# Kernel tuning notes

Measured on AMD Instinct MI355X. Metric: run time of the kernel, lower is better.

Reference implementation:

```python
import jax, jax.numpy as jnp
import numpy as np

N_NODES = 50000
N_EDGES = 800000
VOCAB = 4096
EMB = 128
HID = 128


def glorot(key, shape):
    limit = float(np.sqrt(6.0 / (shape[0] + shape[1])))
    return jax.random.uniform(key, shape, jnp.float32, -limit, limit)


def setup_inputs() -> dict:
    key = jax.random.key(0)
    k = jax.random.split(key, 6)
    x = jax.random.randint(k[0], (N_NODES, 1), 0, VOCAB, dtype=jnp.int64)
    edge_index = jax.random.randint(k[1], (2, N_EDGES), 0, N_NODES, dtype=jnp.int64)
    # Embedding init: normal(0, dim^-0.5)
    emb = jax.random.normal(k[2], (VOCAB, EMB), jnp.float32) * (EMB ** -0.5)
    W1 = glorot(k[3], (EMB, 2 * HID))
    b1 = jnp.zeros((2 * HID,), jnp.float32)
    W2 = glorot(k[4], (2 * HID, HID))
    b2 = jnp.zeros((HID,), jnp.float32)
    return {"x": x, "edge_index": edge_index, "emb": emb,
            "W1": W1, "b1": b1, "W2": W2, "b2": b2}


def _gcn_conv(h, src, dst, norm, W, b):
    # PyG GCNConv: transform then degree-normalized aggregate over A + I.
    h = h @ W                                   # [N, F_out]
    msg = norm[:, None] * h[src]                # [(E+N), F_out] gather
    out = jax.ops.segment_sum(msg, dst, num_segments=N_NODES)  # scatter-add
    return out + b


def _edges_with_self_loops_and_norm(edge_index):
    loop = jnp.arange(N_NODES, dtype=edge_index.dtype)
    src = jnp.concatenate([edge_index[0], loop])
    dst = jnp.concatenate([edge_index[1], loop])
    deg = jax.ops.segment_sum(jnp.ones_like(dst, jnp.float32), dst,
                              num_segments=N_NODES)
    inv_sqrt = jnp.where(deg > 0, deg ** -0.5, 0.0)
    norm = inv_sqrt[src] * inv_sqrt[dst]        # [(E+N)]
    return src, dst, norm


def reference(x, edge_index, emb, W1, b1, W2, b2):
    src, dst, norm = _edges_with_self_loops_and_norm(edge_index)
    h = emb[x[:, 0]]                            # embedding lookup + squeeze(1)
    h = jax.nn.relu(_gcn_conv(h, src, dst, norm, W1, b1))
    h = _gcn_conv(h, src, dst, norm, W2, b2)
    return h
```

## Files before the change

kernel.cpp:

```cpp
#include <hip/hip_runtime.h>


constexpr int FEAT = 128;
constexpr int HID2 = 256;
constexpr int CAP  = 64;

typedef __attribute__((ext_vector_type(8))) __bf16 bf16x8;
typedef __attribute__((ext_vector_type(4))) float f32x4;
typedef __attribute__((ext_vector_type(8))) _Float16 f16x8;
union FragU { uint4 u; bf16x8 b; };
union H16 { _Float16 f; unsigned short u; };

__device__ inline void split_bf16_rne(float v, unsigned short& h, unsigned short& l) {
  unsigned u = __float_as_uint(v);
  unsigned short hh = (unsigned short)((u + 0x7FFFu + ((u >> 16) & 1u)) >> 16);
  float r = v - __uint_as_float(((unsigned)hh) << 16);
  unsigned u2 = __float_as_uint(r);
  unsigned short ll = (unsigned short)((u2 + 0x7FFFu + ((u2 >> 16) & 1u)) >> 16);
  h = hh; l = ll;
}

__device__ inline void split_trunc1(float v, unsigned short& h, unsigned short& l) {
  unsigned u = __float_as_uint(v);
  h = (unsigned short)(u >> 16);
  float r = v - __uint_as_float(u & 0xFFFF0000u);
  l = (unsigned short)(__float_as_uint(r) >> 16);
}


__global__ __launch_bounds__(256) void k_init_prep(int* cnt, int N, int nblkN,
    const float* __restrict__ W1, const float* __restrict__ W2,
    unsigned short* __restrict__ w1s_hi, unsigned short* __restrict__ w1s_lo,
    unsigned short* __restrict__ w2s_hi, unsigned short* __restrict__ w2s_lo) {
  int b = blockIdx.x;
  if (b < nblkN) {
    int i = b * 256 + threadIdx.x;
    if (i < N) cnt[i] = 0;
    return;
  }
  int idx = (b - nblkN) * 256 + threadIdx.x;
  unsigned short h, l;
  if (idx < FEAT * HID2) {
    int k = idx >> 8, n = idx & 255;
    split_bf16_rne(W1[idx], h, l);
    int t = n >> 4, lr = n & 15, kc = k >> 5, quad = (k >> 3) & 3, j = k & 7;
    int us = (((t * 4 + kc) * 64 + quad * 16 + lr) << 3) + j;
    w1s_hi[us] = h;
    w1s_lo[us] = l;
  } else {
    int jj = idx - FEAT * HID2;
    int k = jj >> 7, n = jj & 127;
    split_bf16_rne(W2[jj], h, l);
    int t = n >> 4, lr = n & 15, kc = k >> 5, quad = (k >> 3) & 3, j = k & 7;
    int us = (((t * 8 + kc) * 64 + quad * 16 + lr) << 3) + j;
    w2s_hi[us] = h;
    w2s_lo[us] = l;
  }
}


__global__ __launch_bounds__(256) void k_bucket(const int* __restrict__ src,
    const int* __restrict__ dst, int* cnt, unsigned short* csr, int E, int chunkN) {
  int g = blockIdx.x & 7;
  int e = (blockIdx.x >> 3) * 256 + threadIdx.x;
  if (e >= E) return;
  int d = dst[e];
  int lo = g * chunkN;
  if (d >= lo && d < lo + chunkN) {
    int pos = atomicAdd(&cnt[d], 1);
    if (pos < CAP) csr[d * CAP + pos] = (unsigned short)src[e];
  }
}


__global__ __launch_bounds__(512, 2) void k_gmlp(
    const int* __restrict__ x, const float* __restrict__ emb,
    const int* __restrict__ cnt, const unsigned short* __restrict__ csr,
    const uint4* __restrict__ w1s_hi, const uint4* __restrict__ w1s_lo,
    const uint4* __restrict__ w2s_hi, const uint4* __restrict__ w2s_lo,
    const float* __restrict__ b1,
    unsigned short* __restrict__ hs2h, int N, int Np) {
  __shared__ __align__(16) unsigned short h1h[32 * 256];
  __shared__ __align__(16) unsigned short h1l[32 * 256];
  unsigned short* aggh = h1h;
  unsigned short* aggl = h1l;

  int tid  = threadIdx.x;
  int wave = tid >> 6, lane = tid & 63, quad = lane >> 4, lr = lane & 15;
  int bid  = blockIdx.x;
  int m0 = bid * 32;
  int rot1 = bid & 1;
  int kh0  = (bid >> 1) & 1;

  int glr = tid >> 4;
  int rt_g = glr >> 4, r15 = glr & 15;
  int c4  = (tid & 15) * 4;
  int kcg = c4 >> 5, qdg = (c4 >> 3) & 3, sub = c4 & 7;
  int L   = qdg * 16 + r15;
  int posL = L ^ ((L >> 4) & 3);

  {
    int node = m0 + glr;
    int fA = rt_g * 4 + kcg, fB = fA + 2;
    int pos = posL ^ ((fA & 1) << 2);
    int usA = ((fA * 64 + pos) << 3) + sub;
    int usB = ((fB * 64 + pos) << 3) + sub;
    if (node < N) {
      int degN = cnt[node];
      float wd = rsqrtf((float)(degN + 1));
      int deg = degN > CAP ? CAP : degN;

      const float* e0 = &emb[(long long)x[node] * FEAT + c4];
      float4 aA = *reinterpret_cast<const float4*>(e0);
      float4 aB = *reinterpret_cast<const float4*>(e0 + 64);
      aA.x *= wd; aA.y *= wd; aA.z *= wd; aA.w *= wd;
      aB.x *= wd; aB.y *= wd; aB.z *= wd; aB.w *= wd;

      const unsigned short* row = csr + node * CAP;
      int j = 0;
      for (; j + 7 < deg; j += 8) {
        uint4 c8 = *reinterpret_cast<const uint4*>(row + j);
        int s[8] = {(int)(c8.x & 0xFFFF), (int)(c8.x >> 16),
                    (int)(c8.y & 0xFFFF), (int)(c8.y >> 16),
                    (int)(c8.z & 0xFFFF), (int)(c8.z >> 16),
                    (int)(c8.w & 0xFFFF), (int)(c8.w >> 16)};
        const float* p[8];
        #pragma unroll
        for (int q = 0; q < 8; ++q) p[q] = &emb[(long long)x[s[q]] * FEAT + c4];
        float ws[8];
        #pragma unroll
        for (int q = 0; q < 8; ++q) ws[q] = rsqrtf((float)(cnt[s[q]] + 1));
        float4 rA[8], rB[8];
        #pragma unroll
        for (int q = 0; q < 8; ++q) {
          rA[q] = *reinterpret_cast<const float4*>(p[q]);
          rB[q] = *reinterpret_cast<const float4*>(p[q] + 64);
        }
        #pragma unroll
        for (int q = 0; q < 8; ++q) {
          aA.x += ws[q] * rA[q].x; aA.y += ws[q] * rA[q].y;
          aA.z += ws[q] * rA[q].z; aA.w += ws[q] * rA[q].w;
          aB.x += ws[q] * rB[q].x; aB.y += ws[q] * rB[q].y;
          aB.z += ws[q] * rB[q].z; aB.w += ws[q] * rB[q].w;
        }
      }
      if (j + 3 < deg) {
        uint2 c4e = *reinterpret_cast<const uint2*>(row + j);
        int s[4] = {(int)(c4e.x & 0xFFFF), (int)(c4e.x >> 16),
                    (int)(c4e.y & 0xFFFF), (int)(c4e.y >> 16)};
        const float* p[4];
        #pragma unroll
        for (int q = 0; q < 4; ++q) p[q] = &emb[(long long)x[s[q]] * FEAT + c4];
        float ws[4];
        #pragma unroll
        for (int q = 0; q < 4; ++q) ws[q] = rsqrtf((float)(cnt[s[q]] + 1));
        float4 rA[4], rB[4];
        #pragma unroll
        for (int q = 0; q < 4; ++q) {
          rA[q] = *reinterpret_cast<const float4*>(p[q]);
          rB[q] = *reinterpret_cast<const float4*>(p[q] + 64);
        }
        #pragma unroll
        for (int q = 0; q < 4; ++q) {
          aA.x += ws[q] * rA[q].x; aA.y += ws[q] * rA[q].y;
          aA.z += ws[q] * rA[q].z; aA.w += ws[q] * rA[q].w;
          aB.x += ws[q] * rB[q].x; aB.y += ws[q] * rB[q].y;
          aB.z += ws[q] * rB[q].z; aB.w += ws[q] * rB[q].w;
        }
        j += 4;
      }
      for (; j < deg; ++j) {
        int s = row[j];
        float w = rsqrtf((float)(cnt[s] + 1));
        const float* p = &emb[(long long)x[s] * FEAT + c4];
        float4 a = *reinterpret_cast<const float4*>(p);
        float4 b = *reinterpret_cast<const float4*>(p + 64);
        aA.x += w * a.x; aA.y += w * a.y; aA.z += w * a.z; aA.w += w * a.w;
        aB.x += w * b.x; aB.y += w * b.y; aB.z += w * b.z; aB.w += w * b.w;
      }

      aA.x *= wd; aA.y *= wd; aA.z *= wd; aA.w *= wd;
      aB.x *= wd; aB.y *= wd; aB.z *= wd; aB.w *= wd;
      ushort4 hA, lA, hB, lB;
      split_bf16_rne(aA.x, hA.x, lA.x);
      split_bf16_rne(aA.y, hA.y, lA.y);
      split_bf16_rne(aA.z, hA.z, lA.z);
      split_bf16_rne(aA.w, hA.w, lA.w);
      split_bf16_rne(aB.x, hB.x, lB.x);
      split_bf16_rne(aB.y, hB.y, lB.y);
      split_bf16_rne(aB.z, hB.z, lB.z);
      split_bf16_rne(aB.w, hB.w, lB.w);
      *reinterpret_cast<ushort4*>(aggh + usA) = hA;
      *reinterpret_cast<ushort4*>(aggl + usA) = lA;
      *reinterpret_cast<ushort4*>(aggh + usB) = hB;
      *reinterpret_cast<ushort4*>(aggl + usB) = lB;
    } else {
      ushort4 z = {0, 0, 0, 0};
      *reinterpret_cast<ushort4*>(aggh + usA) = z;
      *reinterpret_cast<ushort4*>(aggl + usA) = z;
      *reinterpret_cast<ushort4*>(aggh + usB) = z;
      *reinterpret_cast<ushort4*>(aggl + usB) = z;
    }
  }

  FragU bh[2][4], bl[2][4];
  auto loadB1 = [&](int t, int buf) {
    #pragma unroll
    for (int kc = 0; kc < 4; ++kc) {
      bh[buf][kc].u = w1s_hi[(t * 4 + kc) * 64 + lane];
      bl[buf][kc].u = w1s_lo[(t * 4 + kc) * 64 + lane];
    }
  };
  int t0 = wave * 2;
  loadB1(t0 + rot1, 0);

  __syncthreads();

  FragU a1h[2][4], a1l[2][4];
  {
    int posR = lane ^ ((lane >> 4) & 3);
    #pragma unroll
    for (int rt = 0; rt < 2; ++rt)
      #pragma unroll
      for (int kc = 0; kc < 4; ++kc) {
        int f = rt * 4 + kc;
        int us = ((f * 64 + (posR ^ ((f & 1) << 2))) << 3);
        a1h[rt][kc].u = *reinterpret_cast<const uint4*>(aggh + us);
        a1l[rt][kc].u = *reinterpret_cast<const uint4*>(aggl + us);
      }
  }

  __syncthreads();

  auto comp1 = [&](int t, int buf) {
    f32x4 hh[2], hl[2], lh[2];
    #pragma unroll
    for (int rt = 0; rt < 2; ++rt) {
      hh[rt] = f32x4{0.f, 0.f, 0.f, 0.f};
      hl[rt] = f32x4{0.f, 0.f, 0.f, 0.f};
      lh[rt] = f32x4{0.f, 0.f, 0.f, 0.f};
    }
    #pragma unroll
    for (int kc = 0; kc < 4; ++kc)
      #pragma unroll
      for (int rt = 0; rt < 2; ++rt) {
        hh[rt] = __builtin_amdgcn_mfma_f32_16x16x32_bf16(a1h[rt][kc].b, bh[buf][kc].b, hh[rt], 0, 0, 0);
        hl[rt] = __builtin_amdgcn_mfma_f32_16x16x32_bf16(a1h[rt][kc].b, bl[buf][kc].b, hl[rt], 0, 0, 0);
        lh[rt] = __builtin_amdgcn_mfma_f32_16x16x32_bf16(a1l[rt][kc].b, bh[buf][kc].b, lh[rt], 0, 0, 0);
      }
    float bias = b1[t * 16 + lr];
    int c = t * 2 + (lr >> 3), jj = lr & 7;
    #pragma unroll
    for (int rt = 0; rt < 2; ++rt)
      #pragma unroll
      for (int r = 0; r < 4; ++r) {
        float v = hh[rt][r] + hl[rt][r] + lh[rt][r] + bias;
        v = v > 0.f ? v : 0.f;
        int row = rt * 16 + quad * 4 + r;
        int us = ((row * 32 + (c ^ (row & 7))) << 3) + jj;
        unsigned short sh, sl;
        split_trunc1(v, sh, sl);
        h1h[us] = sh;
        h1l[us] = sl;
      }
  };

  #pragma unroll
  for (int i = 0; i < 2; ++i) {
    if (i < 1) loadB1(t0 + ((i + 1 + rot1) & 1), 1);
    comp1(t0 + ((i + rot1) & 1), i & 1);
  }

  float inv_r[2][4];
  #pragma unroll
  for (int rt = 0; rt < 2; ++rt)
    #pragma unroll
    for (int r = 0; r < 4; ++r) {
      int gg = m0 + rt * 16 + quad * 4 + r;
      inv_r[rt][r] = rsqrtf((float)(cnt[gg < N ? gg : N - 1] + 1));
    }

  int t2 = wave;
  FragU pb2h[4], pb2l[4];
  #pragma unroll
  for (int kc = 0; kc < 4; ++kc) {
    pb2h[kc].u = w2s_hi[(t2 * 8 + kh0 * 4 + kc) * 64 + lane];
    pb2l[kc].u = w2s_lo[(t2 * 8 + kh0 * 4 + kc) * 64 + lane];
  }

  __syncthreads();

  {
    f32x4 hh[2], hl[2], lh[2];
    #pragma unroll
    for (int rt = 0; rt < 2; ++rt) {
      hh[rt] = f32x4{0.f, 0.f, 0.f, 0.f};
      hl[rt] = f32x4{0.f, 0.f, 0.f, 0.f};
      lh[rt] = f32x4{0.f, 0.f, 0.f, 0.f};
    }
    #pragma unroll
    for (int khi = 0; khi < 2; ++khi) {
      int kh = kh0 ^ khi;
      FragU b2h[4], b2l[4];
      if (khi == 0) {
        #pragma unroll
        for (int kc = 0; kc < 4; ++kc) { b2h[kc] = pb2h[kc]; b2l[kc] = pb2l[kc]; }
      } else {
        #pragma unroll
        for (int kc = 0; kc < 4; ++kc) {
          b2h[kc].u = w2s_hi[(t2 * 8 + kh * 4 + kc) * 64 + lane];
          b2l[kc].u = w2s_lo[(t2 * 8 + kh * 4 + kc) * 64 + lane];
        }
      }
      FragU a2h[2][4], a2l[2][4];
      #pragma unroll
      for (int rt = 0; rt < 2; ++rt) {
        int row = rt * 16 + lr;
        #pragma unroll
        for (int kc = 0; kc < 4; ++kc) {
          int pc = (kh * 16 + kc * 4 + quad) ^ (row & 7);
          a2h[rt][kc].u = *reinterpret_cast<const uint4*>(&h1h[(row * 32 + pc) << 3]);
          a2l[rt][kc].u = *reinterpret_cast<const uint4*>(&h1l[(row * 32 + pc) << 3]);
        }
      }
      #pragma unroll
      for (int kc = 0; kc < 4; ++kc)
        #pragma unroll
        for (int rt = 0; rt < 2; ++rt) {
          hh[rt] = __builtin_amdgcn_mfma_f32_16x16x32_bf16(a2h[rt][kc].b, b2h[kc].b, hh[rt], 0, 0, 0);
          hl[rt] = __builtin_amdgcn_mfma_f32_16x16x32_bf16(a2h[rt][kc].b, b2l[kc].b, hl[rt], 0, 0, 0);
          lh[rt] = __builtin_amdgcn_mfma_f32_16x16x32_bf16(a2l[rt][kc].b, b2h[kc].b, lh[rt], 0, 0, 0);
        }
    }
    unsigned short* sl2 = hs2h + (long long)(t2 >> 2) * Np * 64 + (t2 & 3) * 16;
    #pragma unroll
    for (int rt = 0; rt < 2; ++rt)
      #pragma unroll
      for (int r = 0; r < 4; ++r) {
        int gg = m0 + rt * 16 + quad * 4 + r;
        if (gg < N) {
          float v = (hh[rt][r] + hl[rt][r] + lh[rt][r]) * inv_r[rt][r];
          H16 cv;
          cv.f = (_Float16)v;
          sl2[(long long)gg * 64 + lr] = cv.u;
        }
      }
  }
}


__global__ __launch_bounds__(256) void k_gather_l2(
    const unsigned short* __restrict__ hs2h,
    const int* __restrict__ cnt, const unsigned short* __restrict__ csr,
    const float* __restrict__ bias, float* __restrict__ out, int N, int Np) {
  int g    = blockIdx.x & 7;
  int half = g >> 2, qtr = g & 3;
  int Nq   = (N + 3) >> 2;
  int local = (blockIdx.x >> 3) * 32 + (threadIdx.x >> 3);
  if (local >= Nq) return;
  int node = qtr * Nq + local;
  if (node >= N) return;
  int f8 = (threadIdx.x & 7) * 8;
  const unsigned short* sl = hs2h + (long long)half * Np * 64;

  f32x4 a0, a1;
  {
    f16x8 v = *reinterpret_cast<const f16x8*>(sl + (long long)node * 64 + f8);
    a0 = __builtin_convertvector(__builtin_shufflevector(v, v, 0, 1, 2, 3), f32x4);
    a1 = __builtin_convertvector(__builtin_shufflevector(v, v, 4, 5, 6, 7), f32x4);
  }

  const unsigned short* row = csr + node * CAP;
  int degN = cnt[node];
  int deg = degN > CAP ? CAP : degN;
  int j = 0;
  for (; j + 15 < deg; j += 16) {
    uint4 c0 = *reinterpret_cast<const uint4*>(row + j);
    uint4 c1 = *reinterpret_cast<const uint4*>(row + j + 8);
    int s[16] = {(int)(c0.x & 0xFFFF), (int)(c0.x >> 16),
                 (int)(c0.y & 0xFFFF), (int)(c0.y >> 16),
                 (int)(c0.z & 0xFFFF), (int)(c0.z >> 16),
                 (int)(c0.w & 0xFFFF), (int)(c0.w >> 16),
                 (int)(c1.x & 0xFFFF), (int)(c1.x >> 16),
                 (int)(c1.y & 0xFFFF), (int)(c1.y >> 16),
                 (int)(c1.z & 0xFFFF), (int)(c1.z >> 16),
                 (int)(c1.w & 0xFFFF), (int)(c1.w >> 16)};
    f16x8 r[16];
    #pragma unroll
    for (int q = 0; q < 16; ++q)
      r[q] = *reinterpret_cast<const f16x8*>(sl + (long long)s[q] * 64 + f8);
    #pragma unroll
    for (int q = 0; q < 16; ++q) {
      a0 += __builtin_convertvector(__builtin_shufflevector(r[q], r[q], 0, 1, 2, 3), f32x4);
      a1 += __builtin_convertvector(__builtin_shufflevector(r[q], r[q], 4, 5, 6, 7), f32x4);
    }
  }
  if (j + 7 < deg) {
    uint4 c8 = *reinterpret_cast<const uint4*>(row + j);
    int s[8] = {(int)(c8.x & 0xFFFF), (int)(c8.x >> 16),
                (int)(c8.y & 0xFFFF), (int)(c8.y >> 16),
                (int)(c8.z & 0xFFFF), (int)(c8.z >> 16),
                (int)(c8.w & 0xFFFF), (int)(c8.w >> 16)};
    f16x8 r[8];
    #pragma unroll
    for (int q = 0; q < 8; ++q)
      r[q] = *reinterpret_cast<const f16x8*>(sl + (long long)s[q] * 64 + f8);
    #pragma unroll
    for (int q = 0; q < 8; ++q) {
      a0 += __builtin_convertvector(__builtin_shufflevector(r[q], r[q], 0, 1, 2, 3), f32x4);
      a1 += __builtin_convertvector(__builtin_shufflevector(r[q], r[q], 4, 5, 6, 7), f32x4);
    }
    j += 8;
  }
  if (j + 3 < deg) {
    uint2 c4e = *reinterpret_cast<const uint2*>(row + j);
    int s[4] = {(int)(c4e.x & 0xFFFF), (int)(c4e.x >> 16),
                (int)(c4e.y & 0xFFFF), (int)(c4e.y >> 16)};
    f16x8 r[4];
    #pragma unroll
    for (int q = 0; q < 4; ++q)
      r[q] = *reinterpret_cast<const f16x8*>(sl + (long long)s[q] * 64 + f8);
    #pragma unroll
    for (int q = 0; q < 4; ++q) {
      a0 += __builtin_convertvector(__builtin_shufflevector(r[q], r[q], 0, 1, 2, 3), f32x4);
      a1 += __builtin_convertvector(__builtin_shufflevector(r[q], r[q], 4, 5, 6, 7), f32x4);
    }
    j += 4;
  }
  for (; j < deg; ++j) {
    f16x8 v = *reinterpret_cast<const f16x8*>(sl + (long long)row[j] * 64 + f8);
    a0 += __builtin_convertvector(__builtin_shufflevector(v, v, 0, 1, 2, 3), f32x4);
    a1 += __builtin_convertvector(__builtin_shufflevector(v, v, 4, 5, 6, 7), f32x4);
  }

  float w = rsqrtf((float)(degN + 1));
  int col = half * 64 + f8;
  f32x4 b0 = *reinterpret_cast<const f32x4*>(&bias[col]);
  f32x4 b1v = *reinterpret_cast<const f32x4*>(&bias[col + 4]);
  a0 = a0 * w + b0;
  a1 = a1 * w + b1v;
  *reinterpret_cast<f32x4*>(&out[(long long)node * FEAT + col]) = a0;
  *reinterpret_cast<f32x4*>(&out[(long long)node * FEAT + col + 4]) = a1;
}


extern "C" void kernel_launch(void* const* d_in, const int* in_sizes, int n_in,
                              void* d_out, int out_size, void* d_ws, size_t ws_size,
                              hipStream_t stream) {
  const int*   x   = (const int*)d_in[0];
  const int*   ei  = (const int*)d_in[1];
  const float* emb = (const float*)d_in[2];
  const float* W1  = (const float*)d_in[3];
  const float* b1  = (const float*)d_in[4];
  const float* W2  = (const float*)d_in[5];
  const float* b2  = (const float*)d_in[6];
  float* out = (float*)d_out;

  const int N  = in_sizes[0];
  const int E  = in_sizes[1] / 2;
  const int nblk_mlp = (N + 31) / 32;
  const int Np = nblk_mlp * 32;
  const int chunkN = (N + 7) / 8;
  const int* src = ei;
  const int* dst = ei + E;

  int* cnt = (int*)d_ws;
  unsigned short* csr = (unsigned short*)(cnt + N);
  unsigned short* hs2h = csr + (long long)N * CAP;
  unsigned short* w1s_hi = hs2h + (long long)Np * FEAT;
  unsigned short* w1s_lo = w1s_hi + FEAT * HID2;
  unsigned short* w2s_hi = w1s_lo + FEAT * HID2;
  unsigned short* w2s_lo = w2s_hi + FEAT * HID2;

  const int Nq = (N + 3) / 4;
  const int nblk_N  = (N + 255) / 256;
  const int nblk_E8 = ((E + 255) / 256) * 8;
  const int nblk_g2 = ((Nq + 31) / 32) * 8;

  k_init_prep<<<nblk_N + 256, 256, 0, stream>>>(cnt, N, nblk_N, W1, W2,
                                                w1s_hi, w1s_lo, w2s_hi, w2s_lo);
  k_bucket<<<nblk_E8, 256, 0, stream>>>(src, dst, cnt, csr, E, chunkN);

  k_gmlp<<<nblk_mlp, 512, 0, stream>>>(x, emb, cnt, csr,
                                       (const uint4*)w1s_hi, (const uint4*)w1s_lo,
                                       (const uint4*)w2s_hi, (const uint4*)w2s_lo,
                                       b1, hs2h, N, Np);
  k_gather_l2<<<nblk_g2, 256, 0, stream>>>(hs2h, cnt, csr, b2, out, N, Np);
}
```

Measured before the change: 209.8 us.

## Pack node token, clamped degree and inverse-sqrt norm into one record; vectorize bucketing

Adds a small kernel that precomputes, per node, a packed 8-byte record holding the token id, the clamped degree and rsqrt(deg+1). The aggregation and gather kernels now read that single record per neighbor instead of separate x and cnt loads plus an rsqrt. The edge bucketing kernel gets an int4-vectorized variant that processes four edges per thread when E is divisible by 4. It costs an extra launch and workspace space, and packs the token id into 16 bits, which assumes the vocabulary fits in 16 bits.

```diff
diff --git a/kernel.cpp b/kernel.cpp
--- a/kernel.cpp
+++ b/kernel.cpp
@@ -59,6 +59,26 @@
 }
 
 
+__global__ __launch_bounds__(256) void k_bucket4(const int* __restrict__ src,
+    const int* __restrict__ dst, int* cnt, unsigned short* csr, int E, int chunkN) {
+  int g = blockIdx.x & 7;
+  int lo = g * chunkN, hi = lo + chunkN;
+  int e4 = ((blockIdx.x >> 3) * 256 + threadIdx.x) * 4;
+  if (e4 >= E) return;
+  int4 d4 = *reinterpret_cast<const int4*>(dst + e4);
+  bool m0 = d4.x >= lo && d4.x < hi;
+  bool m1 = d4.y >= lo && d4.y < hi;
+  bool m2 = d4.z >= lo && d4.z < hi;
+  bool m3 = d4.w >= lo && d4.w < hi;
+  if (m0 | m1 | m2 | m3) {
+    int4 s4 = *reinterpret_cast<const int4*>(src + e4);
+    if (m0) { int p = atomicAdd(&cnt[d4.x], 1); if (p < CAP) csr[d4.x * CAP + p] = (unsigned short)s4.x; }
+    if (m1) { int p = atomicAdd(&cnt[d4.y], 1); if (p < CAP) csr[d4.y * CAP + p] = (unsigned short)s4.y; }
+    if (m2) { int p = atomicAdd(&cnt[d4.z], 1); if (p < CAP) csr[d4.z * CAP + p] = (unsigned short)s4.z; }
+    if (m3) { int p = atomicAdd(&cnt[d4.w], 1); if (p < CAP) csr[d4.w * CAP + p] = (unsigned short)s4.w; }
+  }
+}
+
 __global__ __launch_bounds__(256) void k_bucket(const int* __restrict__ src,
     const int* __restrict__ dst, int* cnt, unsigned short* csr, int E, int chunkN) {
   int g = blockIdx.x & 7;
@@ -73,9 +93,22 @@
 }
 
 
+__global__ __launch_bounds__(256) void k_xinv(const int* __restrict__ x,
+    const int* __restrict__ cnt, uint2* __restrict__ xi, int N) {
+  int i = blockIdx.x * 256 + threadIdx.x;
+  if (i >= N) return;
+  int c = cnt[i];
+  int mc = c > CAP ? CAP : c;
+  uint2 r;
+  r.x = (unsigned)x[i] | ((unsigned)mc << 16);
+  r.y = __float_as_uint(rsqrtf((float)(c + 1)));
+  xi[i] = r;
+}
+
+
 __global__ __launch_bounds__(512, 2) void k_gmlp(
-    const int* __restrict__ x, const float* __restrict__ emb,
-    const int* __restrict__ cnt, const unsigned short* __restrict__ csr,
+    const uint2* __restrict__ xi, const float* __restrict__ emb,
+    const unsigned short* __restrict__ csr,
     const uint4* __restrict__ w1s_hi, const uint4* __restrict__ w1s_lo,
     const uint4* __restrict__ w2s_hi, const uint4* __restrict__ w2s_lo,
     const float* __restrict__ b1,
@@ -106,11 +139,11 @@
     int usA = ((fA * 64 + pos) << 3) + sub;
     int usB = ((fB * 64 + pos) << 3) + sub;
     if (node < N) {
-      int degN = cnt[node];
-      float wd = rsqrtf((float)(degN + 1));
-      int deg = degN > CAP ? CAP : degN;
-
-      const float* e0 = &emb[(long long)x[node] * FEAT + c4];
+      uint2 rn = xi[node];
+      int deg = (int)(rn.x >> 16);
+      float wd = __uint_as_float(rn.y);
+
+      const float* e0 = &emb[(long long)(rn.x & 0xFFFF) * FEAT + c4];
       float4 aA = *reinterpret_cast<const float4*>(e0);
       float4 aB = *reinterpret_cast<const float4*>(e0 + 64);
       aA.x *= wd; aA.y *= wd; aA.z *= wd; aA.w *= wd;
@@ -124,12 +157,13 @@
                     (int)(c8.y & 0xFFFF), (int)(c8.y >> 16),
                     (int)(c8.z & 0xFFFF), (int)(c8.z >> 16),
                     (int)(c8.w & 0xFFFF), (int)(c8.w >> 16)};
+        uint2 rr[8];
+        #pragma unroll
+        for (int q = 0; q < 8; ++q) rr[q] = xi[s[q]];
         const float* p[8];
         #pragma unroll
-        for (int q = 0; q < 8; ++q) p[q] = &emb[(long long)x[s[q]] * FEAT + c4];
-        float ws[8];
-        #pragma unroll
-        for (int q = 0; q < 8; ++q) ws[q] = rsqrtf((float)(cnt[s[q]] + 1));
+        for (int q = 0; q < 8; ++q)
+          p[q] = &emb[(long long)(rr[q].x & 0xFFFF) * FEAT + c4];
         float4 rA[8], rB[8];
         #pragma unroll
         for (int q = 0; q < 8; ++q) {
@@ -138,22 +172,24 @@
         }
         #pragma unroll
         for (int q = 0; q < 8; ++q) {
-          aA.x += ws[q] * rA[q].x; aA.y += ws[q] * rA[q].y;
-          aA.z += ws[q] * rA[q].z; aA.w += ws[q] * rA[q].w;
-          aB.x += ws[q] * rB[q].x; aB.y += ws[q] * rB[q].y;
-          aB.z += ws[q] * rB[q].z; aB.w += ws[q] * rB[q].w;
+          float w = __uint_as_float(rr[q].y);
+          aA.x += w * rA[q].x; aA.y += w * rA[q].y;
+          aA.z += w * rA[q].z; aA.w += w * rA[q].w;
+          aB.x += w * rB[q].x; aB.y += w * rB[q].y;
+          aB.z += w * rB[q].z; aB.w += w * rB[q].w;
         }
       }
       if (j + 3 < deg) {
         uint2 c4e = *reinterpret_cast<const uint2*>(row + j);
         int s[4] = {(int)(c4e.x & 0xFFFF), (int)(c4e.x >> 16),
                     (int)(c4e.y & 0xFFFF), (int)(c4e.y >> 16)};
+        uint2 rr[4];
+        #pragma unroll
+        for (int q = 0; q < 4; ++q) rr[q] = xi[s[q]];
         const float* p[4];
         #pragma unroll
-        for (int q = 0; q < 4; ++q) p[q] = &emb[(long long)x[s[q]] * FEAT + c4];
-        float ws[4];
-        #pragma unroll
-        for (int q = 0; q < 4; ++q) ws[q] = rsqrtf((float)(cnt[s[q]] + 1));
+        for (int q = 0; q < 4; ++q)
+          p[q] = &emb[(long long)(rr[q].x & 0xFFFF) * FEAT + c4];
         float4 rA[4], rB[4];
         #pragma unroll
         for (int q = 0; q < 4; ++q) {
@@ -162,17 +198,19 @@
         }
         #pragma unroll
         for (int q = 0; q < 4; ++q) {
-          aA.x += ws[q] * rA[q].x; aA.y += ws[q] * rA[q].y;
-          aA.z += ws[q] * rA[q].z; aA.w += ws[q] * rA[q].w;
-          aB.x += ws[q] * rB[q].x; aB.y += ws[q] * rB[q].y;
-          aB.z += ws[q] * rB[q].z; aB.w += ws[q] * rB[q].w;
+          float w = __uint_as_float(rr[q].y);
+          aA.x += w * rA[q].x; aA.y += w * rA[q].y;
+          aA.z += w * rA[q].z; aA.w += w * rA[q].w;
+          aB.x += w * rB[q].x; aB.y += w * rB[q].y;
+          aB.z += w * rB[q].z; aB.w += w * rB[q].w;
         }
         j += 4;
       }
       for (; j < deg; ++j) {
         int s = row[j];
-        float w = rsqrtf((float)(cnt[s] + 1));
-        const float* p = &emb[(long long)x[s] * FEAT + c4];
+        uint2 rr = xi[s];
+        float w = __uint_as_float(rr.y);
+        const float* p = &emb[(long long)(rr.x & 0xFFFF) * FEAT + c4];
         float4 a = *reinterpret_cast<const float4*>(p);
         float4 b = *reinterpret_cast<const float4*>(p + 64);
         aA.x += w * a.x; aA.y += w * a.y; aA.z += w * a.z; aA.w += w * a.w;
@@ -277,7 +315,7 @@
     #pragma unroll
     for (int r = 0; r < 4; ++r) {
       int gg = m0 + rt * 16 + quad * 4 + r;
-      inv_r[rt][r] = rsqrtf((float)(cnt[gg < N ? gg : N - 1] + 1));
+      inv_r[rt][r] = __uint_as_float(xi[gg < N ? gg : N - 1].y);
     }
 
   int t2 = wave;
@@ -351,7 +389,7 @@
 
 __global__ __launch_bounds__(256) void k_gather_l2(
     const unsigned short* __restrict__ hs2h,
-    const int* __restrict__ cnt, const unsigned short* __restrict__ csr,
+    const uint2* __restrict__ xi, const unsigned short* __restrict__ csr,
     const float* __restrict__ bias, float* __restrict__ out, int N, int Np) {
   int g    = blockIdx.x & 7;
   int half = g >> 2, qtr = g & 3;
@@ -371,8 +409,8 @@
   }
 
   const unsigned short* row = csr + node * CAP;
-  int degN = cnt[node];
-  int deg = degN > CAP ? CAP : degN;
+  uint2 rn = xi[node];
+  int deg = (int)(rn.x >> 16);
   int j = 0;
   for (; j + 15 < deg; j += 16) {
     uint4 c0 = *reinterpret_cast<const uint4*>(row + j);
@@ -433,7 +471,7 @@
     a1 += __builtin_convertvector(__builtin_shufflevector(v, v, 4, 5, 6, 7), f32x4);
   }
 
-  float w = rsqrtf((float)(degN + 1));
+  float w = __uint_as_float(rn.y);
   int col = half * 64 + f8;
   f32x4 b0 = *reinterpret_cast<const f32x4*>(&bias[col]);
   f32x4 b1v = *reinterpret_cast<const f32x4*>(&bias[col + 4]);
@@ -471,19 +509,27 @@
   unsigned short* w1s_lo = w1s_hi + FEAT * HID2;
   unsigned short* w2s_hi = w1s_lo + FEAT * HID2;
   unsigned short* w2s_lo = w2s_hi + FEAT * HID2;
+  uintptr_t xi_addr = ((uintptr_t)(w2s_lo + FEAT * HID2) + 7) & ~(uintptr_t)7;
+  uint2* xi = (uint2*)xi_addr;
 
   const int Nq = (N + 3) / 4;
   const int nblk_N  = (N + 255) / 256;
-  const int nblk_E8 = ((E + 255) / 256) * 8;
   const int nblk_g2 = ((Nq + 31) / 32) * 8;
 
   k_init_prep<<<nblk_N + 256, 256, 0, stream>>>(cnt, N, nblk_N, W1, W2,
                                                 w1s_hi, w1s_lo, w2s_hi, w2s_lo);
-  k_bucket<<<nblk_E8, 256, 0, stream>>>(src, dst, cnt, csr, E, chunkN);
-
-  k_gmlp<<<nblk_mlp, 512, 0, stream>>>(x, emb, cnt, csr,
+  if ((E & 3) == 0) {
+    const int nblk_E4 = ((E / 4 + 255) / 256) * 8;
+    k_bucket4<<<nblk_E4, 256, 0, stream>>>(src, dst, cnt, csr, E, chunkN);
+  } else {
+    const int nblk_E8 = ((E + 255) / 256) * 8;
+    k_bucket<<<nblk_E8, 256, 0, stream>>>(src, dst, cnt, csr, E, chunkN);
+  }
+  k_xinv<<<nblk_N, 256, 0, stream>>>(x, cnt, xi, N);
+
+  k_gmlp<<<nblk_mlp, 512, 0, stream>>>(xi, emb, csr,
                                        (const uint4*)w1s_hi, (const uint4*)w1s_lo,
                                        (const uint4*)w2s_hi, (const uint4*)w2s_lo,
                                        b1, hs2h, N, Np);
-  k_gather_l2<<<nblk_g2, 256, 0, stream>>>(hs2h, cnt, csr, b2, out, N, Np);
-}
+  k_gather_l2<<<nblk_g2, 256, 0, stream>>>(hs2h, xi, csr, b2, out, N, Np);
+}
```

After: 216.1 us. 1.03x slower.
